# Optimization experiments

Hardware: AMD Instinct MI355X
Metric: run time of the kernel (lower is better)

## Reference

```python
import jax, jax.numpy as jnp
import numpy as np

LABEL_SIZE = 64
START = LABEL_SIZE - 2
STOP = LABEL_SIZE - 1
NEG = -10000.0


def setup_inputs() -> dict:
    key = jax.random.key(0)
    k1, k2 = jax.random.split(key)
    B, T, L = 512, 512, LABEL_SIZE
    emissions = jax.random.normal(k1, (B, T, L), dtype=jnp.float32)
    # xavier-uniform-ish init, then mask row START (nothing transitions INTO start
    # ... actually transitions[next, prev]: row START = transitions into START)
    bound = float(np.sqrt(6.0 / (L + L)))
    trans = jax.random.uniform(k2, (L, L), dtype=jnp.float32, minval=-bound, maxval=bound)
    trans = trans.at[START, :].set(NEG)   # never transition to START
    trans = trans.at[:, STOP].set(NEG)    # never transition from STOP
    return {"input": emissions, "transitions": trans}


def reference(input, transitions):
    # input: [B, T, L] emission scores; transitions[next_tag, prev_tag]: [L, L]
    B, T, L = input.shape
    init = jnp.full((B, L), NEG, dtype=input.dtype).at[:, START].set(0.0)

    def step(forward_var, emit_t):
        # forward_var: [B, L] (over prev tag); emit_t: [B, L] (over next tag)
        # scores[b, next, prev] = forward_var[b, prev] + transitions[next, prev]
        nv = jax.nn.logsumexp(forward_var[:, None, :] + transitions[None, :, :], axis=-1)
        return nv + emit_t, None

    forward_var, _ = jax.lax.scan(step, init, jnp.swapaxes(input, 0, 1))  # scan over T
    terminal = forward_var + transitions[STOP][None, :]
    return jax.nn.logsumexp(terminal, axis=-1)  # [B] log partition function
```

## Files before the change

### kernel.cpp

```cpp
#include <hip/hip_runtime.h>

#define NTAG 64
#define TLEN 512
#define HALF (TLEN / 2)
#define START_TAG 62
#define STOP_TAG 63
#define CHUNK 32

typedef float v2f __attribute__((ext_vector_type(2)));

__global__ __launch_bounds__(128) void crf_fwd_bwd(
    const float* __restrict__ emis,
    const float* __restrict__ trans,
    float* __restrict__ out)
{
    const int b    = blockIdx.x;
    const int tid  = threadIdx.x;
    const int lane = tid & 63;
    const int w    = tid >> 6;

    __shared__ float lds[2 * 2 * CHUNK * NTAG];
    __shared__ __align__(16) float xst[2][NTAG];
    __shared__ float shv[2][NTAG];
    float* xs = xst[w];

    const float L2E = 1.4426950408889634f;
    const float LN2 = 0.6931471805599453f;

    v2f E2[NTAG / 2];
    #pragma unroll
    for (int k2 = 0; k2 < NTAG / 2; ++k2) {
        float e0, e1;
        if (w == 0) { e0 = trans[lane * NTAG + 2 * k2];   e1 = trans[lane * NTAG + 2 * k2 + 1]; }
        else        { e0 = trans[(2 * k2) * NTAG + lane]; e1 = trans[(2 * k2 + 1) * NTAG + lane]; }
        v2f p; p.x = exp2f(e0 * L2E); p.y = exp2f(e1 * L2E);
        E2[k2] = p;
    }

    const float* eb = emis + (size_t)b * TLEN * NTAG;

    float4 r0, r1, r2, r3, r4, r5, r6, r7;
    #define LOAD_CHUNK(baseT)                                        \
        do {                                                         \
            const float4* gp = (const float4*)(eb + (baseT) * NTAG); \
            r0 = gp[0 * 64 + lane]; r1 = gp[1 * 64 + lane];          \
            r2 = gp[2 * 64 + lane]; r3 = gp[3 * 64 + lane];          \
            r4 = gp[4 * 64 + lane]; r5 = gp[5 * 64 + lane];          \
            r6 = gp[6 * 64 + lane]; r7 = gp[7 * 64 + lane];          \
        } while (0)
    #define EXP4(v) make_float4(exp2f((v).x * L2E), exp2f((v).y * L2E), \
                                exp2f((v).z * L2E), exp2f((v).w * L2E))
    #define STORE_CHUNK_EXP(bufp)                                    \
        do {                                                         \
            float4* b4 = (float4*)(bufp);                            \
            b4[0 * 64 + lane] = EXP4(r0); b4[1 * 64 + lane] = EXP4(r1); \
            b4[2 * 64 + lane] = EXP4(r2); b4[3 * 64 + lane] = EXP4(r3); \
            b4[4 * 64 + lane] = EXP4(r4); b4[5 * 64 + lane] = EXP4(r5); \
            b4[6 * 64 + lane] = EXP4(r6); b4[7 * 64 + lane] = EXP4(r7); \
        } while (0)

    #define QFMA(xv, j, accA, accB)                                  \
        do { v2f lo_, hi_;                                           \
             lo_.x = (xv).x; lo_.y = (xv).y;                         \
             hi_.x = (xv).z; hi_.y = (xv).w;                         \
             accA = __builtin_elementwise_fma(lo_, E2[2*(j)],   accA); \
             accB = __builtin_elementwise_fma(hi_, E2[2*(j)+1], accB); \
        } while (0)

    #define MATVEC_REF(ssum, d_)                                     \
        do {                                                         \
            const float4* xq_ = (const float4*)xs;                   \
            float4 xv_[16];                                          \
            _Pragma("unroll")                                        \
            for (int j = 0; j < 16; ++j) xv_[j] = xq_[j];            \
            int ef_ = (int)((__float_as_uint(xv_[0].x) >> 23) & 0xffu); \
            d_ = (ef_ == 0) ? 0 : ef_ - 127;                         \
            v2f a0={0.f,0.f}, a1={0.f,0.f}, a2={0.f,0.f}, a3={0.f,0.f};\
            v2f a4={0.f,0.f}, a5={0.f,0.f}, a6={0.f,0.f}, a7={0.f,0.f};\
            QFMA(xv_[0],  0, a0, a1); QFMA(xv_[1],  1, a2, a3);      \
            QFMA(xv_[2],  2, a4, a5); QFMA(xv_[3],  3, a6, a7);      \
            QFMA(xv_[4],  4, a0, a1); QFMA(xv_[5],  5, a2, a3);      \
            QFMA(xv_[6],  6, a4, a5); QFMA(xv_[7],  7, a6, a7);      \
            QFMA(xv_[8],  8, a0, a1); QFMA(xv_[9],  9, a2, a3);      \
            QFMA(xv_[10], 10, a4, a5); QFMA(xv_[11], 11, a6, a7);    \
            QFMA(xv_[12], 12, a0, a1); QFMA(xv_[13], 13, a2, a3);    \
            QFMA(xv_[14], 14, a4, a5); QFMA(xv_[15], 15, a6, a7);    \
            v2f s_ = ((a0 + a1) + (a2 + a3)) + ((a4 + a5) + (a6 + a7)); \
            ssum = s_.x + s_.y;                                      \
        } while (0)

    #define WRITE_STATE(v) (xs[lane] = (v))

    #define STEP(buf, s)                                             \
        do {                                                         \
            float em_ = (buf)[(s) * NTAG + lane];                    \
            float ssum_; int d_;                                     \
            MATVEC_REF(ssum_, d_);                                   \
            off += d_;                                               \
            float rs_ = __uint_as_float((unsigned)(127 - d_) << 23); \
            x = ssum_ * (em_ * rs_);                                 \
            WRITE_STATE(x);                                          \
        } while (0)

    float x   = 0.0f;
    int   off = 0;

    if (w == 0) {
        WRITE_STATE(lane == START_TAG ? 1.0f : 0.0f);

        LOAD_CHUNK(0);
        #pragma clang loop unroll(disable)
        for (int ci = 0; ci < 8; ++ci) {
            float* buf = &lds[(ci & 1) * (CHUNK * NTAG)];
            STORE_CHUNK_EXP(buf);
            if (ci < 7) LOAD_CHUNK((ci + 1) * CHUNK);

            #pragma clang loop unroll_count(4)
            for (int s = 0; s < CHUNK; ++s) STEP(buf, s);
        }
    } else {
        float Sv = exp2f(trans[STOP_TAG * NTAG + lane] * L2E);

        LOAD_CHUNK(HALF + 7 * CHUNK);
        #pragma clang loop unroll(disable)
        for (int i = 0; i < 8; ++i) {
            float* buf = &lds[(2 + (i & 1)) * (CHUNK * NTAG)];
            STORE_CHUNK_EXP(buf);
            if (i < 7) LOAD_CHUNK(HALF + (6 - i) * CHUNK);

            int s0 = CHUNK - 1;
            if (i == 0) {
                WRITE_STATE(Sv * buf[(CHUNK - 1) * NTAG + lane]);
                s0 = CHUNK - 2;
            }
            #pragma clang loop unroll_count(4)
            for (int s = s0; s >= 0; --s) STEP(buf, s);
        }
        {
            float ssum_; int d_;
            MATVEC_REF(ssum_, d_);
            off += d_;
            x = ssum_ * __uint_as_float((unsigned)(127 - d_) << 23);
        }
    }

    shv[w][lane] = log2f(x) + (float)off;
    __syncthreads();

    if (w == 0) {
        float v = shv[0][lane] + shv[1][lane];
        float m = v;
        #pragma unroll
        for (int d = 1; d < 64; d <<= 1) m = fmaxf(m, __shfl_xor(m, d, 64));
        float e = exp2f(v - m);
        #pragma unroll
        for (int d = 1; d < 64; d <<= 1) e += __shfl_xor(e, d, 64);
        if (lane == 0) out[b] = LN2 * (m + log2f(e));
    }
}

extern "C" void kernel_launch(void* const* d_in, const int* in_sizes, int n_in,
                              void* d_out, int out_size, void* d_ws, size_t ws_size,
                              hipStream_t stream) {
    const float* emis  = (const float*)d_in[0];
    const float* trans = (const float*)d_in[1];
    float* out = (float*)d_out;
    (void)in_sizes; (void)n_in; (void)out_size; (void)d_ws; (void)ws_size;
    crf_fwd_bwd<<<512, 128, 0, stream>>>(emis, trans, out);
}
```

Measured before the change: 156.2 us.

## Replace LDS state broadcast with DPP row-rotation matvec in registers

The per-step matrix-vector product no longer writes the 64-element state to shared memory and reads it back as float4. Each lane instead rotates the state across lanes with DPP row-rotate operations and accumulates against transition weights pre-permuted per lane to match the rotation order. This removes the LDS write/read round trip and its latency from the serial recurrence. In exchange it uses scalar FMAs instead of packed v2f FMAs, adds about 64 DPP moves per step, and depends on the assumed semantics of the DPP control 0x134/0x13C across all 64 lanes, which the code probes at runtime through a readfirstlane.

After: 236.6 us. 1.51x slower.

```diff
diff --git a/kernel.cpp b/kernel.cpp
--- a/kernel.cpp
+++ b/kernel.cpp
@@ -6,8 +6,6 @@
 #define START_TAG 62
 #define STOP_TAG 63
 #define CHUNK 32
-
-typedef float v2f __attribute__((ext_vector_type(2)));
 
 __global__ __launch_bounds__(128) void crf_fwd_bwd(
     const float* __restrict__ emis,
@@ -20,22 +18,33 @@
     const int w    = tid >> 6;
 
     __shared__ float lds[2 * 2 * CHUNK * NTAG];
-    __shared__ __align__(16) float xst[2][NTAG];
     __shared__ float shv[2][NTAG];
-    float* xs = xst[w];
 
     const float L2E = 1.4426950408889634f;
     const float LN2 = 0.6931471805599453f;
 
-    v2f E2[NTAG / 2];
+    #define ROL1(v) __uint_as_float(__builtin_amdgcn_update_dpp(              \
+        __float_as_uint(v), __float_as_uint(v), 0x134, 0xf, 0xf, false))
+    #define ROR1(v) __uint_as_float(__builtin_amdgcn_update_dpp(              \
+        __float_as_uint(v), __float_as_uint(v), 0x13C, 0xf, 0xf, false))
+
+    int pr  = __builtin_amdgcn_update_dpp(0, lane, 0x134, 0xf, 0xf, false);
+    int d0  = __builtin_amdgcn_readfirstlane(pr);
+    int sgn = (d0 == 1) ? 1 : -1;
+
+    #define TRV(r, c) ((w == 0) ? trans[(r) * NTAG + (c)] : trans[(c) * NTAG + (r)])
+    float Ea[33], Eb[32];
     #pragma unroll
-    for (int k2 = 0; k2 < NTAG / 2; ++k2) {
-        float e0, e1;
-        if (w == 0) { e0 = trans[lane * NTAG + 2 * k2];   e1 = trans[lane * NTAG + 2 * k2 + 1]; }
-        else        { e0 = trans[(2 * k2) * NTAG + lane]; e1 = trans[(2 * k2 + 1) * NTAG + lane]; }
-        v2f p; p.x = exp2f(e0 * L2E); p.y = exp2f(e1 * L2E);
-        E2[k2] = p;
+    for (int i = 1; i <= 32; ++i) {
+        int ia = (lane + sgn * i) & 63;
+        Ea[i] = exp2f(TRV(lane, ia) * L2E);
     }
+    #pragma unroll
+    for (int i = 1; i <= 31; ++i) {
+        int ib = (lane - sgn * i) & 63;
+        Eb[i] = exp2f(TRV(lane, ib) * L2E);
+    }
+    float Ez = exp2f(TRV(lane, lane) * L2E);
 
     const float* eb = emis + (size_t)b * TLEN * NTAG;
 
@@ -59,54 +68,42 @@
             b4[6 * 64 + lane] = EXP4(r6); b4[7 * 64 + lane] = EXP4(r7); \
         } while (0)
 
-    #define QFMA(xv, j, accA, accB)                                  \
-        do { v2f lo_, hi_;                                           \
-             lo_.x = (xv).x; lo_.y = (xv).y;                         \
-             hi_.x = (xv).z; hi_.y = (xv).w;                         \
-             accA = __builtin_elementwise_fma(lo_, E2[2*(j)],   accA); \
-             accB = __builtin_elementwise_fma(hi_, E2[2*(j)+1], accB); \
+    #define ROTMV(ssum, d_)                                          \
+        do {                                                         \
+            unsigned ref_ = __builtin_amdgcn_readfirstlane(__float_as_uint(x)); \
+            int ef_ = (int)((ref_ >> 23) & 0xffu);                   \
+            d_ = (ef_ == 0) ? 0 : ef_ - 127;                         \
+            float xa_ = x, xb_ = x;                                  \
+            float a0_ = Ez * x, a1_ = 0.f, a2_ = 0.f, a3_ = 0.f;     \
+            _Pragma("unroll")                                        \
+            for (int i_ = 1; i_ <= 31; ++i_) {                       \
+                xa_ = ROL1(xa_);                                     \
+                xb_ = ROR1(xb_);                                     \
+                if (i_ & 1) { a1_ = fmaf(Ea[i_], xa_, a1_);          \
+                              a3_ = fmaf(Eb[i_], xb_, a3_); }        \
+                else        { a2_ = fmaf(Ea[i_], xa_, a2_);          \
+                              a0_ = fmaf(Eb[i_], xb_, a0_); }        \
+            }                                                        \
+            xa_ = ROL1(xa_);                                         \
+            a1_ = fmaf(Ea[32], xa_, a1_);                            \
+            ssum = (a0_ + a1_) + (a2_ + a3_);                        \
         } while (0)
-
-    #define MATVEC_REF(ssum, d_)                                     \
-        do {                                                         \
-            const float4* xq_ = (const float4*)xs;                   \
-            float4 xv_[16];                                          \
-            _Pragma("unroll")                                        \
-            for (int j = 0; j < 16; ++j) xv_[j] = xq_[j];            \
-            int ef_ = (int)((__float_as_uint(xv_[0].x) >> 23) & 0xffu); \
-            d_ = (ef_ == 0) ? 0 : ef_ - 127;                         \
-            v2f a0={0.f,0.f}, a1={0.f,0.f}, a2={0.f,0.f}, a3={0.f,0.f};\
-            v2f a4={0.f,0.f}, a5={0.f,0.f}, a6={0.f,0.f}, a7={0.f,0.f};\
-            QFMA(xv_[0],  0, a0, a1); QFMA(xv_[1],  1, a2, a3);      \
-            QFMA(xv_[2],  2, a4, a5); QFMA(xv_[3],  3, a6, a7);      \
-            QFMA(xv_[4],  4, a0, a1); QFMA(xv_[5],  5, a2, a3);      \
-            QFMA(xv_[6],  6, a4, a5); QFMA(xv_[7],  7, a6, a7);      \
-            QFMA(xv_[8],  8, a0, a1); QFMA(xv_[9],  9, a2, a3);      \
-            QFMA(xv_[10], 10, a4, a5); QFMA(xv_[11], 11, a6, a7);    \
-            QFMA(xv_[12], 12, a0, a1); QFMA(xv_[13], 13, a2, a3);    \
-            QFMA(xv_[14], 14, a4, a5); QFMA(xv_[15], 15, a6, a7);    \
-            v2f s_ = ((a0 + a1) + (a2 + a3)) + ((a4 + a5) + (a6 + a7)); \
-            ssum = s_.x + s_.y;                                      \
-        } while (0)
-
-    #define WRITE_STATE(v) (xs[lane] = (v))
 
     #define STEP(buf, s)                                             \
         do {                                                         \
             float em_ = (buf)[(s) * NTAG + lane];                    \
             float ssum_; int d_;                                     \
-            MATVEC_REF(ssum_, d_);                                   \
+            ROTMV(ssum_, d_);                                        \
             off += d_;                                               \
             float rs_ = __uint_as_float((unsigned)(127 - d_) << 23); \
             x = ssum_ * (em_ * rs_);                                 \
-            WRITE_STATE(x);                                          \
         } while (0)
 
     float x   = 0.0f;
     int   off = 0;
 
     if (w == 0) {
-        WRITE_STATE(lane == START_TAG ? 1.0f : 0.0f);
+        x = (lane == START_TAG) ? 1.0f : 0.0f;
 
         LOAD_CHUNK(0);
         #pragma clang loop unroll(disable)
@@ -130,7 +127,7 @@
 
             int s0 = CHUNK - 1;
             if (i == 0) {
-                WRITE_STATE(Sv * buf[(CHUNK - 1) * NTAG + lane]);
+                x = Sv * buf[(CHUNK - 1) * NTAG + lane];
                 s0 = CHUNK - 2;
             }
             #pragma clang loop unroll_count(4)
@@ -138,7 +135,7 @@
         }
         {
             float ssum_; int d_;
-            MATVEC_REF(ssum_, d_);
+            ROTMV(ssum_, d_);
             off += d_;
             x = ssum_ * __uint_as_float((unsigned)(127 - d_) << 23);
         }
```
